# Optimization experiments

Measured on AMD Instinct MI355X. Metric: run time of the kernel, lower is better.

Reference implementation:

```python
import jax, jax.numpy as jnp
import numpy as np

UNITS = 1024
NCLASS = 8000
BATCH = 4096

def setup_inputs() -> dict:
    key = jax.random.key(0)
    k1, k2, k3, k4 = jax.random.split(key, 4)
    inputs = jax.random.randint(k1, (BATCH, 1), 0, NCLASS, dtype=jnp.int32)
    h_tm1 = jax.random.normal(k2, (BATCH, UNITS), dtype=jnp.float32)
    # orthogonal-ish recurrent kernel (scaled normal is fine for a numeric reference)
    recurrent_kernel = jax.random.normal(k3, (UNITS, 4 * UNITS), dtype=jnp.float32) * (1.0 / np.sqrt(UNITS))
    kernel_c = jax.random.normal(k4, (NCLASS, 4 * UNITS), dtype=jnp.float32) * (1.0 / np.sqrt(NCLASS))
    bias_z = jnp.full((UNITS,), 5.0, dtype=jnp.float32)  # initializer=constant(5)
    bias = jnp.zeros((3 * UNITS,), dtype=jnp.float32)
    return {"inputs": inputs, "h_tm1": h_tm1, "recurrent_kernel": recurrent_kernel,
            "kernel_c": kernel_c, "bias_z": bias_z, "bias": bias}

def reference(inputs, h_tm1, recurrent_kernel, kernel_c, bias_z, bias):
    u = h_tm1.shape[-1]
    ch = inputs[:, 0].astype(jnp.int32)
    # one_hot(ch) @ kernel_c == row gather of kernel_c (identical math, O(1) per row)
    c_proj = kernel_c[ch]                      # [B, 4u]
    cz, cr, ch_, co = (c_proj[:, :u], c_proj[:, u:2*u], c_proj[:, 2*u:3*u], c_proj[:, 3*u:])
    Rz, Rr, Rh, Ro = (recurrent_kernel[:, :u], recurrent_kernel[:, u:2*u],
                      recurrent_kernel[:, 2*u:3*u], recurrent_kernel[:, 3*u:])
    z = jax.nn.sigmoid(h_tm1 @ Rz + cz + bias_z)
    r = jax.nn.sigmoid(h_tm1 @ Rr + cr + bias[:u])
    hh = jnp.tanh((r * h_tm1) @ Rh + ch_ + bias[u:2*u])
    h = z * h_tm1 + (1.0 - z) * hh
    o = jnp.tanh(h @ Ro + co + bias[2*u:])
    return (o, h)
```

## Files before the change

### kernel.cpp

```cpp
#include <hip/hip_runtime.h>
#include <stdint.h>

#define UNITS 1024
#define BATCH 4096
#define FOURU 4096

typedef __bf16 bf16x8 __attribute__((ext_vector_type(8)));
typedef float f32x4 __attribute__((ext_vector_type(4)));

__device__ __forceinline__ uint16_t f2bf(float f) {
  uint32_t u = __builtin_bit_cast(uint32_t, f);
  u += 0x7FFFu + ((u >> 16) & 1u);
  return (uint16_t)(u >> 16);
}
__device__ __forceinline__ float bf2f(uint16_t b) {
  uint32_t u = ((uint32_t)b) << 16;
  return __builtin_bit_cast(float, u);
}
__device__ __forceinline__ float fsig(float x) {
  return 1.0f / (1.0f + __expf(-x));
}
__device__ __forceinline__ f32x4 mfma16x16x32(bf16x8 a, bf16x8 b, f32x4 c) {
  return __builtin_amdgcn_mfma_f32_16x16x32_bf16(a, b, c, 0, 0, 0);
}

__device__ __forceinline__ void gll16(uint16_t* lds, const uint16_t* g) {
  __builtin_amdgcn_global_load_lds(
      (const __attribute__((address_space(1))) uint32_t*)g,
      (__attribute__((address_space(3))) uint32_t*)lds, 16, 0, 0);
}

template <int NG>
__device__ __forceinline__ void stage(const uint16_t* __restrict__ src,
                                      uint16_t* lds, int tid) {
  const int wb = tid & 192;
#pragma unroll
  for (int p = 0; p < NG / 256; ++p) {
    const int gi = p * 256 + tid;
    gll16(lds + (p * 256 + wb) * 8, src + (gi >> 2) * UNITS + (gi & 3) * 8);
  }
}

__global__ __launch_bounds__(256) void convert_kernel(const float* __restrict__ in,
                                                      uint16_t* __restrict__ out) {
  const int i = (blockIdx.x * 256 + threadIdx.x) * 4;
  float4 v = *(const float4*)(in + i);
  ushort4 o;
  o.x = f2bf(v.x); o.y = f2bf(v.y); o.z = f2bf(v.z); o.w = f2bf(v.w);
  *(ushort4*)(out + i) = o;
}

__global__ __launch_bounds__(256) void transpose_kernel(const float* __restrict__ R,
                                                        uint16_t* __restrict__ RT) {
  __shared__ float t[32][33];
  const int n0 = blockIdx.x * 32, k0 = blockIdx.y * 32;
  const int tx = threadIdx.x & 31, ty = threadIdx.x >> 5;
#pragma unroll
  for (int i = 0; i < 4; ++i)
    t[ty + i * 8][tx] = R[(k0 + ty + i * 8) * FOURU + n0 + tx];
  __syncthreads();
#pragma unroll
  for (int i = 0; i < 4; ++i)
    RT[(n0 + ty + i * 8) * UNITS + k0 + tx] = f2bf(t[tx][ty + i * 8]);
}

__global__ __launch_bounds__(256) void s1_kernel(
    const uint16_t* __restrict__ hbf, const uint16_t* __restrict__ rt,
    const int* __restrict__ idx, const float* __restrict__ kc,
    const float* __restrict__ bz, const float* __restrict__ bias,
    uint16_t* __restrict__ zb, uint16_t* __restrict__ rhb) {
  __shared__ uint16_t sA[2][512 * 8];
  __shared__ uint16_t sBz[2][256 * 8];
  __shared__ uint16_t sBr[2][256 * 8];
  const int tid = threadIdx.x;
  const int lane = tid & 63, wave = tid >> 6;
  const int l15 = lane & 15, l4 = lane >> 4;
  const int row0 = blockIdx.y * 128, col0 = blockIdx.x * 64;
  const int rb = (wave >> 1) * 64, cb = (wave & 1) * 32;

  const uint16_t* pa = hbf + row0 * UNITS;
  const uint16_t* pbz = rt + col0 * UNITS;
  const uint16_t* pbr = rt + (UNITS + col0) * UNITS;

  f32x4 accZ[4][2] = {};
  f32x4 accR[4][2] = {};

  stage<512>(pa, sA[0], tid);
  stage<256>(pbz, sBz[0], tid);
  stage<256>(pbr, sBr[0], tid);
  __syncthreads();

  int cur = 0;
  for (int k0 = 0; k0 < UNITS; k0 += 32) {
    if (k0 + 32 < UNITS) {
      stage<512>(pa + k0 + 32, sA[cur ^ 1], tid);
      stage<256>(pbz + k0 + 32, sBz[cur ^ 1], tid);
      stage<256>(pbr + k0 + 32, sBr[cur ^ 1], tid);
    }
    const bf16x8* A8 = (const bf16x8*)sA[cur];
    const bf16x8* Bz8 = (const bf16x8*)sBz[cur];
    const bf16x8* Br8 = (const bf16x8*)sBr[cur];
    bf16x8 af[4], bzf[2], brf[2];
#pragma unroll
    for (int m = 0; m < 4; ++m) af[m] = A8[(rb + m * 16 + l15) * 4 + l4];
#pragma unroll
    for (int n = 0; n < 2; ++n) {
      bzf[n] = Bz8[(cb + n * 16 + l15) * 4 + l4];
      brf[n] = Br8[(cb + n * 16 + l15) * 4 + l4];
    }
#pragma unroll
    for (int m = 0; m < 4; ++m)
#pragma unroll
      for (int n = 0; n < 2; ++n) {
        accZ[m][n] = mfma16x16x32(af[m], bzf[n], accZ[m][n]);
        accR[m][n] = mfma16x16x32(af[m], brf[n], accR[m][n]);
      }
    __syncthreads();
    cur ^= 1;
  }

#pragma unroll
  for (int m = 0; m < 4; ++m) {
#pragma unroll
    for (int q = 0; q < 4; ++q) {
      const int i = row0 + rb + m * 16 + l4 * 4 + q;
      const int ch = idx[i];
      const float* kcrow = kc + ch * FOURU;
#pragma unroll
      for (int n = 0; n < 2; ++n) {
        const int j = col0 + cb + n * 16 + l15;
        const int ij = i * UNITS + j;
        float z = fsig(accZ[m][n][q] + kcrow[j] + bz[j]);
        float r = fsig(accR[m][n][q] + kcrow[UNITS + j] + bias[j]);
        float hv = bf2f(hbf[ij]);
        zb[ij] = f2bf(z);
        rhb[ij] = f2bf(r * hv);
      }
    }
  }
}

template <int MODE>
__global__ __launch_bounds__(256) void s23_kernel(
    const uint16_t* __restrict__ abf, const uint16_t* __restrict__ bt,
    const int* __restrict__ idx, const float* __restrict__ kc,
    const float* __restrict__ bias, const float* __restrict__ h32,
    const uint16_t* __restrict__ zb, float* __restrict__ out32,
    uint16_t* __restrict__ outbf) {
  __shared__ uint16_t sA[2][512 * 8];
  __shared__ uint16_t sB[2][256 * 8];
  const int tid = threadIdx.x;
  const int lane = tid & 63, wave = tid >> 6;
  const int l15 = lane & 15, l4 = lane >> 4;
  const int row0 = blockIdx.y * 128, col0 = blockIdx.x * 64;
  const int rb = (wave >> 1) * 64, cb = (wave & 1) * 32;
  const uint16_t* pa = abf + row0 * UNITS;
  const uint16_t* pb = bt + col0 * UNITS;
  f32x4 acc[4][2] = {};

  stage<512>(pa, sA[0], tid);
  stage<256>(pb, sB[0], tid);
  __syncthreads();

  int cur = 0;
  for (int k0 = 0; k0 < UNITS; k0 += 32) {
    if (k0 + 32 < UNITS) {
      stage<512>(pa + k0 + 32, sA[cur ^ 1], tid);
      stage<256>(pb + k0 + 32, sB[cur ^ 1], tid);
    }
    const bf16x8* A8 = (const bf16x8*)sA[cur];
    const bf16x8* B8 = (const bf16x8*)sB[cur];
    bf16x8 af[4], bff[2];
#pragma unroll
    for (int m = 0; m < 4; ++m) af[m] = A8[(rb + m * 16 + l15) * 4 + l4];
#pragma unroll
    for (int n = 0; n < 2; ++n) bff[n] = B8[(cb + n * 16 + l15) * 4 + l4];
#pragma unroll
    for (int m = 0; m < 4; ++m)
#pragma unroll
      for (int n = 0; n < 2; ++n)
        acc[m][n] = mfma16x16x32(af[m], bff[n], acc[m][n]);
    __syncthreads();
    cur ^= 1;
  }

#pragma unroll
  for (int m = 0; m < 4; ++m) {
#pragma unroll
    for (int q = 0; q < 4; ++q) {
      const int i = row0 + rb + m * 16 + l4 * 4 + q;
      const int ch = idx[i];
      const float* kcrow = kc + ch * FOURU;
#pragma unroll
      for (int n = 0; n < 2; ++n) {
        const int j = col0 + cb + n * 16 + l15;
        const int ij = i * UNITS + j;
        if (MODE == 0) {
          float hh = tanhf(acc[m][n][q] + kcrow[2 * UNITS + j] + bias[UNITS + j]);
          float z = bf2f(zb[ij]);
          float hv = h32[ij];
          float hn = z * hv + (1.0f - z) * hh;
          out32[ij] = hn;
          outbf[ij] = f2bf(hn);
        } else {
          float o = tanhf(acc[m][n][q] + kcrow[3 * UNITS + j] + bias[2 * UNITS + j]);
          out32[ij] = o;
        }
      }
    }
  }
}

extern "C" void kernel_launch(void* const* d_in, const int* in_sizes, int n_in,
                              void* d_out, int out_size, void* d_ws, size_t ws_size,
                              hipStream_t stream) {
  const int* idx = (const int*)d_in[0];
  const float* h32 = (const float*)d_in[1];
  const float* R = (const float*)d_in[2];
  const float* kc = (const float*)d_in[3];
  const float* bz = (const float*)d_in[4];
  const float* bias = (const float*)d_in[5];

  float* o_out = (float*)d_out;
  float* h_out = o_out + (size_t)BATCH * UNITS;

  uint16_t* hbf = (uint16_t*)d_ws;
  uint16_t* rt = hbf + (size_t)BATCH * UNITS;
  uint16_t* rhb = rt + (size_t)FOURU * UNITS;
  uint16_t* hnb = rhb + (size_t)BATCH * UNITS;
  uint16_t* zbuf = hnb + (size_t)BATCH * UNITS;

  convert_kernel<<<dim3(BATCH * UNITS / 1024), 256, 0, stream>>>(h32, hbf);
  transpose_kernel<<<dim3(FOURU / 32, UNITS / 32), 256, 0, stream>>>(R, rt);
  s1_kernel<<<dim3(UNITS / 64, BATCH / 128), 256, 0, stream>>>(
      hbf, rt, idx, kc, bz, bias, zbuf, rhb);
  s23_kernel<0><<<dim3(UNITS / 64, BATCH / 128), 256, 0, stream>>>(
      rhb, rt + (size_t)2 * UNITS * UNITS, idx, kc, bias, h32, zbuf, h_out, hnb);
  s23_kernel<1><<<dim3(UNITS / 64, BATCH / 128), 256, 0, stream>>>(
      hnb, rt + (size_t)3 * UNITS * UNITS, idx, kc, bias, nullptr, nullptr, o_out, nullptr);
}
```

Measured before the change: 121.3 us.

## Unify GEMM kernels with 64-wide K tiles and merge prep kernels

Merges the bf16 convert and transpose kernels into one launch. Replaces the three GEMM stages with one templated kernel that stages 64-wide K slices, halving the number of loop iterations and barriers. The first stage now treats the z and r gates as one contiguous 128-column N tile and splits the epilogue by column, and reads r*h from the fp32 h instead of the bf16 copy. It also adds a two-blocks-per-SM launch bound, at the cost of double the LDS per block and more register pressure.

```diff
diff --git a/kernel.cpp b/kernel.cpp
--- a/kernel.cpp
+++ b/kernel.cpp
@@ -30,91 +30,93 @@
       (__attribute__((address_space(3))) uint32_t*)lds, 16, 0, 0);
 }
 
-template <int NG>
-__device__ __forceinline__ void stage(const uint16_t* __restrict__ src,
-                                      uint16_t* lds, int tid) {
+template <int ROWS>
+__device__ __forceinline__ void stage64(const uint16_t* __restrict__ src,
+                                        uint16_t* lds, int tid) {
   const int wb = tid & 192;
 #pragma unroll
-  for (int p = 0; p < NG / 256; ++p) {
+  for (int p = 0; p < ROWS / 32; ++p) {
     const int gi = p * 256 + tid;
-    gll16(lds + (p * 256 + wb) * 8, src + (gi >> 2) * UNITS + (gi & 3) * 8);
+    const int h = gi / (ROWS * 4);
+    const int r = (gi >> 2) & (ROWS - 1);
+    const int kg = gi & 3;
+    gll16(lds + (p * 256 + wb) * 8, src + r * UNITS + h * 32 + kg * 8);
   }
 }
 
-__global__ __launch_bounds__(256) void convert_kernel(const float* __restrict__ in,
-                                                      uint16_t* __restrict__ out) {
-  const int i = (blockIdx.x * 256 + threadIdx.x) * 4;
-  float4 v = *(const float4*)(in + i);
-  ushort4 o;
-  o.x = f2bf(v.x); o.y = f2bf(v.y); o.z = f2bf(v.z); o.w = f2bf(v.w);
-  *(ushort4*)(out + i) = o;
+__global__ __launch_bounds__(256) void prep_kernel(const float* __restrict__ h32,
+                                                   uint16_t* __restrict__ hbf,
+                                                   const float* __restrict__ R,
+                                                   uint16_t* __restrict__ RT) {
+  __shared__ float t[32][33];
+  const int b = blockIdx.x;
+  if (b < 4096) {
+    const int i = (b * 256 + threadIdx.x) * 4;
+    float4 v = *(const float4*)(h32 + i);
+    ushort4 o;
+    o.x = f2bf(v.x); o.y = f2bf(v.y); o.z = f2bf(v.z); o.w = f2bf(v.w);
+    *(ushort4*)(hbf + i) = o;
+  } else {
+    const int bb = b - 4096;
+    const int n0 = (bb & 127) * 32, k0 = (bb >> 7) * 32;
+    const int tx = threadIdx.x & 31, ty = threadIdx.x >> 5;
+#pragma unroll
+    for (int i = 0; i < 4; ++i)
+      t[ty + i * 8][tx] = R[(size_t)(k0 + ty + i * 8) * FOURU + n0 + tx];
+    __syncthreads();
+#pragma unroll
+    for (int i = 0; i < 4; ++i)
+      RT[(size_t)(n0 + ty + i * 8) * UNITS + k0 + tx] = f2bf(t[tx][ty + i * 8]);
+  }
 }
 
-__global__ __launch_bounds__(256) void transpose_kernel(const float* __restrict__ R,
-                                                        uint16_t* __restrict__ RT) {
-  __shared__ float t[32][33];
-  const int n0 = blockIdx.x * 32, k0 = blockIdx.y * 32;
-  const int tx = threadIdx.x & 31, ty = threadIdx.x >> 5;
-#pragma unroll
-  for (int i = 0; i < 4; ++i)
-    t[ty + i * 8][tx] = R[(k0 + ty + i * 8) * FOURU + n0 + tx];
-  __syncthreads();
-#pragma unroll
-  for (int i = 0; i < 4; ++i)
-    RT[(n0 + ty + i * 8) * UNITS + k0 + tx] = f2bf(t[tx][ty + i * 8]);
-}
-
-__global__ __launch_bounds__(256) void s1_kernel(
-    const uint16_t* __restrict__ hbf, const uint16_t* __restrict__ rt,
+template <int BN, int EPI>
+__global__ __launch_bounds__(256, 2) void gemm_kernel(
+    const uint16_t* __restrict__ abf, const uint16_t* __restrict__ bt,
     const int* __restrict__ idx, const float* __restrict__ kc,
     const float* __restrict__ bz, const float* __restrict__ bias,
-    uint16_t* __restrict__ zb, uint16_t* __restrict__ rhb) {
-  __shared__ uint16_t sA[2][512 * 8];
-  __shared__ uint16_t sBz[2][256 * 8];
-  __shared__ uint16_t sBr[2][256 * 8];
+    const float* __restrict__ h32, const uint16_t* __restrict__ zb_in,
+    float* __restrict__ out32, uint16_t* __restrict__ outbf,
+    uint16_t* __restrict__ out2bf) {
+  constexpr int NF = BN / 32;
+  __shared__ uint16_t sA[2][128 * 64];
+  __shared__ uint16_t sB[2][BN * 64];
   const int tid = threadIdx.x;
   const int lane = tid & 63, wave = tid >> 6;
   const int l15 = lane & 15, l4 = lane >> 4;
-  const int row0 = blockIdx.y * 128, col0 = blockIdx.x * 64;
-  const int rb = (wave >> 1) * 64, cb = (wave & 1) * 32;
+  const int row0 = blockIdx.y * 128, col0 = blockIdx.x * BN;
+  const int rb = (wave >> 1) * 64, cb = (wave & 1) * (BN / 2);
+  const uint16_t* pa = abf + (size_t)row0 * UNITS;
+  const uint16_t* pb = bt + (size_t)col0 * UNITS;
+  f32x4 acc[4][NF] = {};
 
-  const uint16_t* pa = hbf + row0 * UNITS;
-  const uint16_t* pbz = rt + col0 * UNITS;
-  const uint16_t* pbr = rt + (UNITS + col0) * UNITS;
-
-  f32x4 accZ[4][2] = {};
-  f32x4 accR[4][2] = {};
-
-  stage<512>(pa, sA[0], tid);
-  stage<256>(pbz, sBz[0], tid);
-  stage<256>(pbr, sBr[0], tid);
+  stage64<128>(pa, sA[0], tid);
+  stage64<BN>(pb, sB[0], tid);
   __syncthreads();
 
   int cur = 0;
-  for (int k0 = 0; k0 < UNITS; k0 += 32) {
-    if (k0 + 32 < UNITS) {
-      stage<512>(pa + k0 + 32, sA[cur ^ 1], tid);
-      stage<256>(pbz + k0 + 32, sBz[cur ^ 1], tid);
-      stage<256>(pbr + k0 + 32, sBr[cur ^ 1], tid);
+  for (int t = 0; t < UNITS / 64; ++t) {
+    if (t < UNITS / 64 - 1) {
+      stage64<128>(pa + (t + 1) * 64, sA[cur ^ 1], tid);
+      stage64<BN>(pb + (t + 1) * 64, sB[cur ^ 1], tid);
     }
     const bf16x8* A8 = (const bf16x8*)sA[cur];
-    const bf16x8* Bz8 = (const bf16x8*)sBz[cur];
-    const bf16x8* Br8 = (const bf16x8*)sBr[cur];
-    bf16x8 af[4], bzf[2], brf[2];
+    const bf16x8* B8 = (const bf16x8*)sB[cur];
 #pragma unroll
-    for (int m = 0; m < 4; ++m) af[m] = A8[(rb + m * 16 + l15) * 4 + l4];
+    for (int h = 0; h < 2; ++h) {
+      bf16x8 af[4], bf[NF];
 #pragma unroll
-    for (int n = 0; n < 2; ++n) {
-      bzf[n] = Bz8[(cb + n * 16 + l15) * 4 + l4];
-      brf[n] = Br8[(cb + n * 16 + l15) * 4 + l4];
+      for (int m = 0; m < 4; ++m)
+        af[m] = A8[h * 128 * 4 + (rb + m * 16 + l15) * 4 + l4];
+#pragma unroll
+      for (int n = 0; n < NF; ++n)
+        bf[n] = B8[h * BN * 4 + (cb + n * 16 + l15) * 4 + l4];
+#pragma unroll
+      for (int m = 0; m < 4; ++m)
+#pragma unroll
+        for (int n = 0; n < NF; ++n)
+          acc[m][n] = mfma16x16x32(af[m], bf[n], acc[m][n]);
     }
-#pragma unroll
-    for (int m = 0; m < 4; ++m)
-#pragma unroll
-      for (int n = 0; n < 2; ++n) {
-        accZ[m][n] = mfma16x16x32(af[m], bzf[n], accZ[m][n]);
-        accR[m][n] = mfma16x16x32(af[m], brf[n], accR[m][n]);
-      }
     __syncthreads();
     cur ^= 1;
   }
@@ -125,86 +127,32 @@
     for (int q = 0; q < 4; ++q) {
       const int i = row0 + rb + m * 16 + l4 * 4 + q;
       const int ch = idx[i];
-      const float* kcrow = kc + ch * FOURU;
+      const float* kcrow = kc + (size_t)ch * FOURU;
 #pragma unroll
-      for (int n = 0; n < 2; ++n) {
-        const int j = col0 + cb + n * 16 + l15;
-        const int ij = i * UNITS + j;
-        float z = fsig(accZ[m][n][q] + kcrow[j] + bz[j]);
-        float r = fsig(accR[m][n][q] + kcrow[UNITS + j] + bias[j]);
-        float hv = bf2f(hbf[ij]);
-        zb[ij] = f2bf(z);
-        rhb[ij] = f2bf(r * hv);
-      }
-    }
-  }
-}
-
-template <int MODE>
-__global__ __launch_bounds__(256) void s23_kernel(
-    const uint16_t* __restrict__ abf, const uint16_t* __restrict__ bt,
-    const int* __restrict__ idx, const float* __restrict__ kc,
-    const float* __restrict__ bias, const float* __restrict__ h32,
-    const uint16_t* __restrict__ zb, float* __restrict__ out32,
-    uint16_t* __restrict__ outbf) {
-  __shared__ uint16_t sA[2][512 * 8];
-  __shared__ uint16_t sB[2][256 * 8];
-  const int tid = threadIdx.x;
-  const int lane = tid & 63, wave = tid >> 6;
-  const int l15 = lane & 15, l4 = lane >> 4;
-  const int row0 = blockIdx.y * 128, col0 = blockIdx.x * 64;
-  const int rb = (wave >> 1) * 64, cb = (wave & 1) * 32;
-  const uint16_t* pa = abf + row0 * UNITS;
-  const uint16_t* pb = bt + col0 * UNITS;
-  f32x4 acc[4][2] = {};
-
-  stage<512>(pa, sA[0], tid);
-  stage<256>(pb, sB[0], tid);
-  __syncthreads();
-
-  int cur = 0;
-  for (int k0 = 0; k0 < UNITS; k0 += 32) {
-    if (k0 + 32 < UNITS) {
-      stage<512>(pa + k0 + 32, sA[cur ^ 1], tid);
-      stage<256>(pb + k0 + 32, sB[cur ^ 1], tid);
-    }
-    const bf16x8* A8 = (const bf16x8*)sA[cur];
-    const bf16x8* B8 = (const bf16x8*)sB[cur];
-    bf16x8 af[4], bff[2];
-#pragma unroll
-    for (int m = 0; m < 4; ++m) af[m] = A8[(rb + m * 16 + l15) * 4 + l4];
-#pragma unroll
-    for (int n = 0; n < 2; ++n) bff[n] = B8[(cb + n * 16 + l15) * 4 + l4];
-#pragma unroll
-    for (int m = 0; m < 4; ++m)
-#pragma unroll
-      for (int n = 0; n < 2; ++n)
-        acc[m][n] = mfma16x16x32(af[m], bff[n], acc[m][n]);
-    __syncthreads();
-    cur ^= 1;
-  }
-
-#pragma unroll
-  for (int m = 0; m < 4; ++m) {
-#pragma unroll
-    for (int q = 0; q < 4; ++q) {
-      const int i = row0 + rb + m * 16 + l4 * 4 + q;
-      const int ch = idx[i];
-      const float* kcrow = kc + ch * FOURU;
-#pragma unroll
-      for (int n = 0; n < 2; ++n) {
-        const int j = col0 + cb + n * 16 + l15;
-        const int ij = i * UNITS + j;
-        if (MODE == 0) {
-          float hh = tanhf(acc[m][n][q] + kcrow[2 * UNITS + j] + bias[UNITS + j]);
-          float z = bf2f(zb[ij]);
+      for (int n = 0; n < NF; ++n) {
+        const int jc = col0 + cb + n * 16 + l15;
+        const float a = acc[m][n][q];
+        if (EPI == 0) {
+          if (jc < UNITS) {
+            float z = fsig(a + kcrow[jc] + bz[jc]);
+            outbf[(size_t)i * UNITS + jc] = f2bf(z);
+          } else {
+            const int j = jc - UNITS;
+            const size_t ij = (size_t)i * UNITS + j;
+            float r = fsig(a + kcrow[jc] + bias[j]);
+            out2bf[ij] = f2bf(r * h32[ij]);
+          }
+        } else if (EPI == 1) {
+          const size_t ij = (size_t)i * UNITS + jc;
+          float hh = tanhf(a + kcrow[2 * UNITS + jc] + bias[UNITS + jc]);
+          float z = bf2f(zb_in[ij]);
           float hv = h32[ij];
           float hn = z * hv + (1.0f - z) * hh;
           out32[ij] = hn;
           outbf[ij] = f2bf(hn);
         } else {
-          float o = tanhf(acc[m][n][q] + kcrow[3 * UNITS + j] + bias[2 * UNITS + j]);
-          out32[ij] = o;
+          const size_t ij = (size_t)i * UNITS + jc;
+          out32[ij] = tanhf(a + kcrow[3 * UNITS + jc] + bias[2 * UNITS + jc]);
         }
       }
     }
@@ -230,12 +178,16 @@
   uint16_t* hnb = rhb + (size_t)BATCH * UNITS;
   uint16_t* zbuf = hnb + (size_t)BATCH * UNITS;
 
-  convert_kernel<<<dim3(BATCH * UNITS / 1024), 256, 0, stream>>>(h32, hbf);
-  transpose_kernel<<<dim3(FOURU / 32, UNITS / 32), 256, 0, stream>>>(R, rt);
-  s1_kernel<<<dim3(UNITS / 64, BATCH / 128), 256, 0, stream>>>(
-      hbf, rt, idx, kc, bz, bias, zbuf, rhb);
-  s23_kernel<0><<<dim3(UNITS / 64, BATCH / 128), 256, 0, stream>>>(
-      rhb, rt + (size_t)2 * UNITS * UNITS, idx, kc, bias, h32, zbuf, h_out, hnb);
-  s23_kernel<1><<<dim3(UNITS / 64, BATCH / 128), 256, 0, stream>>>(
-      hnb, rt + (size_t)3 * UNITS * UNITS, idx, kc, bias, nullptr, nullptr, o_out, nullptr);
+  prep_kernel<<<dim3(8192), 256, 0, stream>>>(h32, hbf, R, rt);
+
+  gemm_kernel<128, 0><<<dim3(16, 32), 256, 0, stream>>>(
+      hbf, rt, idx, kc, bz, bias, h32, nullptr, nullptr, zbuf, rhb);
+
+  gemm_kernel<64, 1><<<dim3(16, 32), 256, 0, stream>>>(
+      rhb, rt + (size_t)2 * UNITS * UNITS, idx, kc, bz, bias, h32, zbuf,
+      h_out, hnb, nullptr);
+
+  gemm_kernel<64, 2><<<dim3(16, 32), 256, 0, stream>>>(
+      hnb, rt + (size_t)3 * UNITS * UNITS, idx, kc, bz, bias, nullptr, nullptr,
+      o_out, nullptr, nullptr);
 }
```

Result: slower. 136.7 us (+12.7%).
